# Performance work log

Measured on AMD Instinct MI355X. Metric: run time of the kernel, lower is better.

## Reference

```python
import jax, jax.numpy as jnp
import numpy as np

S, B, D, H = 256, 32, 512, 512

def setup_inputs() -> dict:
    key = jax.random.key(0)
    ks = jax.random.split(key, 14)
    return {
        "x": jax.random.normal(ks[0], (S, B, D), jnp.float32),
        "hidden_prev": jax.random.normal(ks[1], (1, B, H), jnp.float32) * 0.1,
        "Z_state": jax.random.normal(ks[2], (1, B, H, D), jnp.float32) * 0.01,
        "F_state": jax.random.normal(ks[3], (1, B, H, D), jnp.float32) * 0.01,
        "wz_state": jax.random.normal(ks[4], (1, B, H), jnp.float32) * 0.01,
        "wf_state": jax.random.normal(ks[5], (1, B, H), jnp.float32) * 0.01,
        "bz_state": jax.random.normal(ks[6], (1, B, H), jnp.float32) * 0.01,
        "bf_state": jax.random.normal(ks[7], (1, B, H), jnp.float32) * 0.01,
        "wm_z": jax.random.normal(ks[8], (H, D), jnp.float32) * 0.1,
        "wm_f": jax.random.normal(ks[9], (H, D), jnp.float32) * 0.1,
        "wv_z": jax.random.normal(ks[10], (1, H), jnp.float32) * 0.1,
        "wv_f": jax.random.normal(ks[11], (1, H), jnp.float32) * 0.1,
        "bias_z": jax.random.normal(ks[12], (1, H), jnp.float32) * 0.1,
        "bias_f": jax.random.normal(ks[13], (1, H), jnp.float32) * 0.1,
    }

def reference(x, hidden_prev, Z_state, F_state, wz_state, wf_state, bz_state, bf_state,
              wm_z, wm_f, wv_z, wv_f, bias_z, bias_f):
    # Input projections for both gates, done once: [S,B,H]
    pre_z = jnp.einsum('sbd,hd->sbh', x, wm_z)
    pre_f = jnp.einsum('sbd,hd->sbh', x, wm_f)

    def step(carry, inp):
        cell, Z, Fm, wz, wf, bz, bf = carry
        x_t, pz, pf = inp  # [B,D], [B,H], [B,H]
        z = jnp.tanh(pz + wv_z * cell + bias_z)          # [B,H]
        f = jax.nn.sigmoid(pf + wv_f * cell + bias_f)    # [B,H]
        zf = (1.0 - f) * (1.0 - z * z)
        fz = (cell - z) * (1.0 - f) * f
        common = f + zf * wv_z + fz * wv_f
        # RTRL sensitivity updates (outer products over [B,H,D])
        Zn = common[..., None] * Z + zf[..., None] * x_t[:, None, :]
        Fn = common[..., None] * Fm + fz[..., None] * x_t[:, None, :]
        wzn = cell * zf + common * wz
        wfn = cell * fz + common * wf
        bzn = zf + common * bz
        bfn = fz + common * bf
        new_cell = cell * f + (1.0 - f) * z
        return (new_cell, Zn, Fn, wzn, wfn, bzn, bfn), new_cell

    carry0 = (hidden_prev[0], Z_state[0], F_state[0],
              wz_state[0], wf_state[0], bz_state[0], bf_state[0])
    carry, cells = jax.lax.scan(step, carry0, (x, pre_z, pre_f))
    new_cell, Zn, Fn, wzn, wfn, bzn, bfn = carry
    return (cells, new_cell[None], Zn[None], Fn[None],
            wzn[None], wfn[None], bzn[None], bfn[None])
```

## Files before the change

kernel.cpp:

```cpp
#include <hip/hip_runtime.h>
#include <hip/hip_bf16.h>
#include <math.h>

namespace {

typedef short short8 __attribute__((ext_vector_type(8)));
typedef float floatx4 __attribute__((ext_vector_type(4)));
typedef unsigned int uint32;
typedef unsigned short u16;
typedef unsigned long long u64;

constexpr int S = 256, B = 32, D = 512, H = 512;
constexpr int BH = B * H;
constexpr int M1 = S * B;
constexpr int SBH = S * BH;

__device__ __forceinline__ int swz(int row, int col8) {
  return row * 64 + (col8 ^ ((row & 7) << 3));
}

__device__ __forceinline__ uint32 pkbf(float lo, float hi) {
  __hip_bfloat162 h = __float22bfloat162_rn(make_float2(lo, hi));
  uint32 r;
  __builtin_memcpy(&r, &h, 4);
  return r;
}

__device__ __forceinline__ float fast_sigmoid(float x) {
  float e = __expf(-x);
  return __builtin_amdgcn_rcpf(1.0f + e);
}
__device__ __forceinline__ float fast_tanh(float x) {
  float e = __expf(-2.0f * x);
  return fmaf(2.0f, __builtin_amdgcn_rcpf(1.0f + e), -1.0f);
}

__global__ __launch_bounds__(256) void proj_gemm(
    const float* __restrict__ x, const float* __restrict__ wmz,
    const float* __restrict__ wmf, float2* __restrict__ pzf) {
  __shared__ u16 As[128 * 64];
  __shared__ u16 Bzs[64 * 64];
  __shared__ u16 Bfs[64 * 64];
  const int tid = threadIdx.x;
  const int m0 = blockIdx.x * 128;
  const int n0 = blockIdx.y * 64;
  const int w = tid >> 6, l = tid & 63;
  const int lr = l & 15, lg = l >> 4;
  floatx4 accz[2][4], accf[2][4];
#pragma unroll
  for (int m = 0; m < 2; ++m)
#pragma unroll
    for (int n = 0; n < 4; ++n) {
      accz[m][n] = 0;
      accf[m][n] = 0;
    }
  const int sr = tid >> 3;
  const int sc = (tid & 7) * 8;
  for (int k0 = 0; k0 < D; k0 += 64) {
    __syncthreads();
#pragma unroll
    for (int p = 0; p < 4; ++p) {
      const int r = sr + 32 * p;
      const float* xp = &x[(size_t)(m0 + r) * D + k0 + sc];
      float4 a = *(const float4*)xp;
      float4 b = *(const float4*)(xp + 4);
      uint4 o;
      o.x = pkbf(a.x, a.y);
      o.y = pkbf(a.z, a.w);
      o.z = pkbf(b.x, b.y);
      o.w = pkbf(b.z, b.w);
      *(uint4*)&As[swz(r, sc)] = o;
    }
#pragma unroll
    for (int p = 0; p < 2; ++p) {
      const int r = sr + 32 * p;
      const float* zp = &wmz[(size_t)(n0 + r) * D + k0 + sc];
      float4 a = *(const float4*)zp;
      float4 b = *(const float4*)(zp + 4);
      uint4 o;
      o.x = pkbf(a.x, a.y);
      o.y = pkbf(a.z, a.w);
      o.z = pkbf(b.x, b.y);
      o.w = pkbf(b.z, b.w);
      *(uint4*)&Bzs[swz(r, sc)] = o;
      const float* fp = &wmf[(size_t)(n0 + r) * D + k0 + sc];
      float4 c = *(const float4*)fp;
      float4 d = *(const float4*)(fp + 4);
      uint4 q;
      q.x = pkbf(c.x, c.y);
      q.y = pkbf(c.z, c.w);
      q.z = pkbf(d.x, d.y);
      q.w = pkbf(d.z, d.w);
      *(uint4*)&Bfs[swz(r, sc)] = q;
    }
    __syncthreads();
    __builtin_amdgcn_s_setprio(1);
#pragma unroll
    for (int kk = 0; kk < 2; ++kk) {
      const int kb = kk * 32 + lg * 8;
      short8 a0 = *(const short8*)&As[swz(32 * w + lr, kb)];
      short8 a1 = *(const short8*)&As[swz(32 * w + 16 + lr, kb)];
#pragma unroll
      for (int n = 0; n < 4; ++n) {
        short8 bz = *(const short8*)&Bzs[swz(16 * n + lr, kb)];
        short8 bf = *(const short8*)&Bfs[swz(16 * n + lr, kb)];
        accz[0][n] = __builtin_amdgcn_mfma_f32_16x16x32_bf16(a0, bz, accz[0][n], 0, 0, 0);
        accz[1][n] = __builtin_amdgcn_mfma_f32_16x16x32_bf16(a1, bz, accz[1][n], 0, 0, 0);
        accf[0][n] = __builtin_amdgcn_mfma_f32_16x16x32_bf16(a0, bf, accf[0][n], 0, 0, 0);
        accf[1][n] = __builtin_amdgcn_mfma_f32_16x16x32_bf16(a1, bf, accf[1][n], 0, 0, 0);
      }
    }
    __builtin_amdgcn_s_setprio(0);
  }
#pragma unroll
  for (int m = 0; m < 2; ++m)
#pragma unroll
    for (int n = 0; n < 4; ++n)
#pragma unroll
      for (int j = 0; j < 4; ++j) {
        int row = m0 + 32 * w + 16 * m + lg * 4 + j;
        int col = n0 + 16 * n + lr;
        pzf[(size_t)row * H + col] = make_float2(accz[m][n][j], accf[m][n][j]);
      }
}

#define STEP_BODY(J)                                                       \
    const float z = fast_tanh(fmaf(wvz, cell, pzv));                       \
    const float f = fast_sigmoid(fmaf(wvf, cell, pfv));                    \
    const float zf = (1.0f - f) * (1.0f - z * z);                          \
    const float fz = (cell - z) * (1.0f - f) * f;                          \
    const float common = f + zf * wvz + fz * wvf;                          \
    wz = fmaf(common, wz, cell * zf);                                      \
    wf = fmaf(common, wf, cell * fz);                                      \
    bz = fmaf(common, bz, zf);                                             \
    bf = fmaf(common, bf, fz);                                             \
    cell = fmaf(f, cell - z, z);                                           \
    const size_t ti = (size_t)(t0 + (J)) * BH;                             \
    cp[ti] = cell;                                                         \
    pz[ti] = make_float2(__uint_as_float(pkbf(zf, fz)), common);

#define STEP_L(J, Q)                                                       \
  {                                                                        \
    const float pzv = Q.x + bsz, pfv = Q.y + bsf;                          \
    Q = pz[(size_t)(t0 + 16 + (J)) * BH];                                  \
    STEP_BODY(J)                                                           \
  }

#define STEP_N(J, Q)                                                       \
  {                                                                        \
    const float pzv = Q.x + bsz, pfv = Q.y + bsf;                          \
    STEP_BODY(J)                                                           \
  }

__global__ __launch_bounds__(64, 1) void scan_fwd(
    const float* __restrict__ hidden_prev, const float* __restrict__ wz0,
    const float* __restrict__ wf0, const float* __restrict__ bz0,
    const float* __restrict__ bf0, const float* __restrict__ wvz_,
    const float* __restrict__ wvf_, const float* __restrict__ bsz_,
    const float* __restrict__ bsf_, float2* pzf_,
    float* __restrict__ out_cells, float* __restrict__ out_newcell,
    float* __restrict__ out_wzn, float* __restrict__ out_wfn,
    float* __restrict__ out_bzn, float* __restrict__ out_bfn) {
  const int bh = blockIdx.x * 64 + threadIdx.x;
  const int h = bh & (H - 1);
  float cell = hidden_prev[bh];
  float wz = wz0[bh], wf = wf0[bh], bz = bz0[bh], bf = bf0[bh];
  const float wvz = wvz_[h], wvf = wvf_[h], bsz = bsz_[h], bsf = bsf_[h];
  float2* pz = pzf_ + bh;
  float* cp = out_cells + bh;

  float2 q0 = pz[(size_t)0 * BH], q1 = pz[(size_t)1 * BH];
  float2 q2 = pz[(size_t)2 * BH], q3 = pz[(size_t)3 * BH];
  float2 q4 = pz[(size_t)4 * BH], q5 = pz[(size_t)5 * BH];
  float2 q6 = pz[(size_t)6 * BH], q7 = pz[(size_t)7 * BH];
  float2 q8 = pz[(size_t)8 * BH], q9 = pz[(size_t)9 * BH];
  float2 q10 = pz[(size_t)10 * BH], q11 = pz[(size_t)11 * BH];
  float2 q12 = pz[(size_t)12 * BH], q13 = pz[(size_t)13 * BH];
  float2 q14 = pz[(size_t)14 * BH], q15 = pz[(size_t)15 * BH];

  for (int t0 = 0; t0 < S - 16; t0 += 16) {
    STEP_L(0, q0)  STEP_L(1, q1)  STEP_L(2, q2)  STEP_L(3, q3)
    STEP_L(4, q4)  STEP_L(5, q5)  STEP_L(6, q6)  STEP_L(7, q7)
    STEP_L(8, q8)  STEP_L(9, q9)  STEP_L(10, q10) STEP_L(11, q11)
    STEP_L(12, q12) STEP_L(13, q13) STEP_L(14, q14) STEP_L(15, q15)
  }
  {
    const int t0 = S - 16;
    STEP_N(0, q0)  STEP_N(1, q1)  STEP_N(2, q2)  STEP_N(3, q3)
    STEP_N(4, q4)  STEP_N(5, q5)  STEP_N(6, q6)  STEP_N(7, q7)
    STEP_N(8, q8)  STEP_N(9, q9)  STEP_N(10, q10) STEP_N(11, q11)
    STEP_N(12, q12) STEP_N(13, q13) STEP_N(14, q14) STEP_N(15, q15)
  }
  out_newcell[bh] = cell;
  out_wzn[bh] = wz;
  out_wfn[bh] = wf;
  out_bzn[bh] = bz;
  out_bfn[bh] = bf;
}

__global__ __launch_bounds__(1024) void suffix_kernel(
    const float2* __restrict__ pzfc, const float* __restrict__ x,
    u16* __restrict__ XT, u16* __restrict__ AzT, u16* __restrict__ AfT,
    float* __restrict__ P0_out) {
  __shared__ union {
    struct {
      float prods[16][65];
      uint32 tl[S * 65];
    } s;
    float xp[4][64][65];
  } u;
  const int tid = threadIdx.x;
  const int bh_l = tid & 63;
  const int c = tid >> 6;

  {
    const int team = tid >> 8;
    const int tt = tid & 255;
    const int tile = blockIdx.x * 4 + team;
    const int b = tile >> 5;
    const int rem = tile & 31;
    const int d0 = (rem >> 2) * 64;
    const int s0 = (rem & 3) * 64;
    const int r = tt >> 4;
    const int c4 = (tt & 15) * 4;
#pragma unroll
    for (int p = 0; p < 4; ++p) {
      const int rr = r + p * 16;
      float4 v = *(const float4*)&x[(size_t)(s0 + rr) * (B * D) +
                                    (size_t)b * D + d0 + c4];
      u.xp[team][c4 + 0][rr] = v.x;
      u.xp[team][c4 + 1][rr] = v.y;
      u.xp[team][c4 + 2][rr] = v.z;
      u.xp[team][c4 + 3][rr] = v.w;
    }
    __syncthreads();
#pragma unroll
    for (int p = 0; p < 4; ++p) {
      const int dr = r + p * 16;
      u64 o = (u64)pkbf(u.xp[team][dr][c4 + 0], u.xp[team][dr][c4 + 1]) |
              ((u64)pkbf(u.xp[team][dr][c4 + 2], u.xp[team][dr][c4 + 3]) << 32);
      *(u64*)&XT[((size_t)b * D + d0 + dr) * S + s0 + c4] = o;
    }
  }
  __syncthreads();

  const int bh = blockIdx.x * 64 + bh_l;
  const float2* p = pzfc + bh;
  float2 v[16];
#pragma unroll
  for (int i = 0; i < 16; ++i) v[i] = p[(size_t)(c * 16 + i) * BH];
  float L = 1.0f;
#pragma unroll
  for (int i = 0; i < 16; ++i) L *= v[i].y;
  u.s.prods[c][bh_l] = L;
  __syncthreads();
  float run = 1.0f;
#pragma unroll
  for (int cc = 1; cc < 16; ++cc)
    if (cc > c) run *= u.s.prods[cc][bh_l];
#pragma unroll
  for (int i = 15; i >= 0; --i) {
    const int t = c * 16 + i;
    const uint32 w32 = __float_as_uint(v[i].x);
    const float zf = __uint_as_float((w32 & 0xffffu) << 16);
    const float fz = __uint_as_float(w32 & 0xffff0000u);
    u.s.tl[t * 65 + bh_l] = pkbf(zf * run, fz * run);
    run *= v[i].y;
  }
  if (c == 0) P0_out[bh] = run;
  __syncthreads();

  const size_t base = (size_t)blockIdx.x * 64 * S;
  const int rot = (bh_l >> 3) & 3;
#pragma unroll
  for (int it = 0; it < 4; ++it) {
    const int qi = it * 1024 + tid;
    const int r = qi >> 6;
    const int qt = (qi & 63) * 4;
    uint32 a[4];
#pragma unroll
    for (int m = 0; m < 4; ++m) {
      const int k = (m + rot) & 3;
      a[k] = u.s.tl[(qt + k) * 65 + r];
    }
    u64 lo = (u64)(a[0] & 0xffffu) | ((u64)(a[1] & 0xffffu) << 16) |
             ((u64)(a[2] & 0xffffu) << 32) | ((u64)(a[3] & 0xffffu) << 48);
    u64 hi = (u64)(a[0] >> 16) | ((u64)(a[1] >> 16) << 16) |
             ((u64)(a[2] >> 16) << 32) | ((u64)(a[3] >> 16) << 48);
    *(u64*)&AzT[base + (size_t)r * S + qt] = lo;
    *(u64*)&AfT[base + (size_t)r * S + qt] = hi;
  }
}

__global__ __launch_bounds__(256, 3) void out_gemm(
    const u16* __restrict__ AzT, const u16* __restrict__ AfT,
    const u16* __restrict__ XT, const float* __restrict__ P0,
    const float* __restrict__ Z0, const float* __restrict__ F0,
    float* __restrict__ Zn, float* __restrict__ Fn) {
  __shared__ u16 smem[2][(128 + 64) * 64];
  const int tid = threadIdx.x;
  const int h0 = blockIdx.x * 128;
  const int d0 = blockIdx.y * 64;
  const int bz = blockIdx.z;
  const int b = bz >> 1;
  const u16* A = ((bz & 1) ? AfT : AzT) + (size_t)b * H * S;
  const float* C0 = (bz & 1) ? F0 : Z0;
  float* Cn = (bz & 1) ? Fn : Zn;
  const u16* Xb = XT + (size_t)b * D * S;
  const int w = tid >> 6, l = tid & 63;
  const int lr = l & 15, lg = l >> 4;
  floatx4 acc[2][4];
#pragma unroll
  for (int m = 0; m < 2; ++m)
#pragma unroll
    for (int n = 0; n < 4; ++n) acc[m][n] = 0;
  const int sr = tid >> 3;
  const int sc = (tid & 7) * 8;

  short8 rA[4], rX[2];

#define OG_LOAD(T0)                                                        \
  {                                                                        \
    _Pragma("unroll") for (int p = 0; p < 4; ++p) {                        \
      const int r = sr + 32 * p;                                           \
      rA[p] = *(const short8*)&A[(size_t)(h0 + r) * S + (T0) + sc];        \
    }                                                                      \
    _Pragma("unroll") for (int p = 0; p < 2; ++p) {                        \
      const int r = sr + 32 * p;                                           \
      rX[p] = *(const short8*)&Xb[(size_t)(d0 + r) * S + (T0) + sc];       \
    }                                                                      \
  }

#define OG_WRITE(BUF)                                                      \
  {                                                                        \
    u16* As_ = smem[BUF];                                                  \
    u16* Xs_ = smem[BUF] + 128 * 64;                                       \
    _Pragma("unroll") for (int p = 0; p < 4; ++p) {                        \
      const int r = sr + 32 * p;                                           \
      *(short8*)&As_[swz(r, sc)] = rA[p];                                  \
    }                                                                      \
    _Pragma("unroll") for (int p = 0; p < 2; ++p) {                        \
      const int r = sr + 32 * p;                                           \
      *(short8*)&Xs_[swz(r, sc)] = rX[p];                                  \
    }                                                                      \
  }

#define OG_COMPUTE(BUF)                                                    \
  {                                                                        \
    const u16* As_ = smem[BUF];                                            \
    const u16* Xs_ = smem[BUF] + 128 * 64;                                 \
    __builtin_amdgcn_s_setprio(1);                                         \
    _Pragma("unroll") for (int kk = 0; kk < 2; ++kk) {                     \
      const int kb = kk * 32 + lg * 8;                                     \
      short8 a0 = *(const short8*)&As_[swz(32 * w + lr, kb)];              \
      short8 a1 = *(const short8*)&As_[swz(32 * w + 16 + lr, kb)];         \
      _Pragma("unroll") for (int n = 0; n < 4; ++n) {                      \
        short8 xf = *(const short8*)&Xs_[swz(16 * n + lr, kb)];            \
        acc[0][n] = __builtin_amdgcn_mfma_f32_16x16x32_bf16(a0, xf, acc[0][n], 0, 0, 0); \
        acc[1][n] = __builtin_amdgcn_mfma_f32_16x16x32_bf16(a1, xf, acc[1][n], 0, 0, 0); \
      }                                                                    \
    }                                                                      \
    __builtin_amdgcn_s_setprio(0);                                         \
  }

  OG_LOAD(0)
  OG_WRITE(0)
  __syncthreads();
  OG_LOAD(64)
  OG_COMPUTE(0)
  OG_WRITE(1)
  __syncthreads();
  OG_LOAD(128)
  OG_COMPUTE(1)
  OG_WRITE(0)
  __syncthreads();
  OG_LOAD(192)
  OG_COMPUTE(0)
  OG_WRITE(1)
  __syncthreads();

  float4 c0v[8];
  float p0v[8];
#pragma unroll
  for (int i = 0; i < 8; ++i) {
    const int id = i * 256 + tid;
    const int row = id >> 4;
    const int c4 = (id & 15) * 4;
    const int h = h0 + row;
    p0v[i] = P0[b * H + h];
    c0v[i] = *(const float4*)&C0[((size_t)b * H + h) * D + d0 + c4];
  }

  OG_COMPUTE(1)

  __syncthreads();
  float* eps = (float*)&smem[0][0];
#pragma unroll
  for (int m = 0; m < 2; ++m)
#pragma unroll
    for (int n = 0; n < 4; ++n)
#pragma unroll
      for (int j = 0; j < 4; ++j) {
        const int row = 32 * w + 16 * m + lg * 4 + j;
        eps[row * 68 + 16 * n + lr] = acc[m][n][j];
      }
  __syncthreads();
#pragma unroll
  for (int i = 0; i < 8; ++i) {
    const int id = i * 256 + tid;
    const int row = id >> 4;
    const int c4 = (id & 15) * 4;
    const int h = h0 + row;
    const size_t gi = ((size_t)b * H + h) * D + d0 + c4;
    const float4 a = *(const float4*)&eps[row * 68 + c4];
    float4 o;
    o.x = fmaf(p0v[i], c0v[i].x, a.x);
    o.y = fmaf(p0v[i], c0v[i].y, a.y);
    o.z = fmaf(p0v[i], c0v[i].z, a.z);
    o.w = fmaf(p0v[i], c0v[i].w, a.w);
    *(float4*)&Cn[gi] = o;
  }
#undef OG_LOAD
#undef OG_WRITE
#undef OG_COMPUTE
}

}

extern "C" void kernel_launch(void* const* d_in, const int* in_sizes, int n_in,
                              void* d_out, int out_size, void* d_ws,
                              size_t ws_size, hipStream_t stream) {
  const float* x = (const float*)d_in[0];
  const float* hidden_prev = (const float*)d_in[1];
  const float* Z_state = (const float*)d_in[2];
  const float* F_state = (const float*)d_in[3];
  const float* wz_state = (const float*)d_in[4];
  const float* wf_state = (const float*)d_in[5];
  const float* bz_state = (const float*)d_in[6];
  const float* bf_state = (const float*)d_in[7];
  const float* wm_z = (const float*)d_in[8];
  const float* wm_f = (const float*)d_in[9];
  const float* wv_z = (const float*)d_in[10];
  const float* wv_f = (const float*)d_in[11];
  const float* bias_z = (const float*)d_in[12];
  const float* bias_f = (const float*)d_in[13];

  float2* pzf = (float2*)d_ws;
  u16* AzT = (u16*)(pzf + SBH);
  u16* AfT = AzT + SBH;
  u16* XT = AfT + SBH;
  float* P0 = (float*)(XT + SBH);

  float* out = (float*)d_out;
  float* out_cells = out;
  float* out_newcell = out + SBH;
  float* out_Zn = out_newcell + BH;
  float* out_Fn = out_Zn + (size_t)BH * D;
  float* out_wzn = out_Fn + (size_t)BH * D;
  float* out_wfn = out_wzn + BH;
  float* out_bzn = out_wfn + BH;
  float* out_bfn = out_bzn + BH;

  proj_gemm<<<dim3(M1 / 128, H / 64), 256, 0, stream>>>(x, wm_z, wm_f, pzf);
  scan_fwd<<<BH / 64, 64, 0, stream>>>(
      hidden_prev, wz_state, wf_state, bz_state, bf_state, wv_z, wv_f, bias_z,
      bias_f, pzf, out_cells, out_newcell, out_wzn, out_wfn, out_bzn,
      out_bfn);
  suffix_kernel<<<BH / 64, 1024, 0, stream>>>(pzf, x, XT, AzT, AfT, P0);
  out_gemm<<<dim3(H / 128, D / 64, B * 2), 256, 0, stream>>>(
      AzT, AfT, XT, P0, Z_state, F_state, out_Zn, out_Fn);
}
```

Before: 102.3 us.

## Single-buffer out_gemm shared memory and split epilogue staging in halves

The out_gemm kernel goes from a double-buffered LDS tile to a single buffer, which halves shared memory per block (about 48KB down to 24KB) and so allows more resident blocks per CU. Because only one buffer remains, an extra barrier is added between compute and the next LDS write, so writes no longer overlap the previous tile's reads. The epilogue now stages the fp32 accumulators through LDS in two 64-row halves so the staging area fits in the smaller buffer. The cost is more __syncthreads and less overlap within each block, traded for higher occupancy.

New measurement: 102.3 us. No clear change (+0.0%).

```diff
diff --git a/kernel.cpp b/kernel.cpp
--- a/kernel.cpp
+++ b/kernel.cpp
@@ -297,7 +297,7 @@
     const u16* __restrict__ XT, const float* __restrict__ P0,
     const float* __restrict__ Z0, const float* __restrict__ F0,
     float* __restrict__ Zn, float* __restrict__ Fn) {
-  __shared__ u16 smem[2][(128 + 64) * 64];
+  __shared__ u16 smem[(128 + 64) * 64];
   const int tid = threadIdx.x;
   const int h0 = blockIdx.x * 128;
   const int d0 = blockIdx.y * 64;
@@ -331,10 +331,10 @@
     }                                                                      \
   }
 
-#define OG_WRITE(BUF)                                                      \
+#define OG_WRITE()                                                         \
   {                                                                        \
-    u16* As_ = smem[BUF];                                                  \
-    u16* Xs_ = smem[BUF] + 128 * 64;                                       \
+    u16* As_ = smem;                                                       \
+    u16* Xs_ = smem + 128 * 64;                                            \
     _Pragma("unroll") for (int p = 0; p < 4; ++p) {                        \
       const int r = sr + 32 * p;                                           \
       *(short8*)&As_[swz(r, sc)] = rA[p];                                  \
@@ -345,10 +345,10 @@
     }                                                                      \
   }
 
-#define OG_COMPUTE(BUF)                                                    \
+#define OG_COMPUTE()                                                       \
   {                                                                        \
-    const u16* As_ = smem[BUF];                                            \
-    const u16* Xs_ = smem[BUF] + 128 * 64;                                 \
+    const u16* As_ = smem;                                                 \
+    const u16* Xs_ = smem + 128 * 64;                                      \
     __builtin_amdgcn_s_setprio(1);                                         \
     _Pragma("unroll") for (int kk = 0; kk < 2; ++kk) {                     \
       const int kb = kk * 32 + lg * 8;                                     \
@@ -364,61 +364,74 @@
   }
 
   OG_LOAD(0)
-  OG_WRITE(0)
+  OG_WRITE()
   __syncthreads();
   OG_LOAD(64)
-  OG_COMPUTE(0)
-  OG_WRITE(1)
+  OG_COMPUTE()
+  __syncthreads();
+  OG_WRITE()
   __syncthreads();
   OG_LOAD(128)
-  OG_COMPUTE(1)
-  OG_WRITE(0)
+  OG_COMPUTE()
+  __syncthreads();
+  OG_WRITE()
   __syncthreads();
   OG_LOAD(192)
-  OG_COMPUTE(0)
-  OG_WRITE(1)
+  OG_COMPUTE()
+  __syncthreads();
+  OG_WRITE()
   __syncthreads();
 
   float4 c0v[8];
   float p0v[8];
 #pragma unroll
-  for (int i = 0; i < 8; ++i) {
-    const int id = i * 256 + tid;
-    const int row = id >> 4;
-    const int c4 = (id & 15) * 4;
-    const int h = h0 + row;
-    p0v[i] = P0[b * H + h];
-    c0v[i] = *(const float4*)&C0[((size_t)b * H + h) * D + d0 + c4];
-  }
-
-  OG_COMPUTE(1)
-
-  __syncthreads();
-  float* eps = (float*)&smem[0][0];
-#pragma unroll
-  for (int m = 0; m < 2; ++m)
-#pragma unroll
-    for (int n = 0; n < 4; ++n)
-#pragma unroll
-      for (int j = 0; j < 4; ++j) {
-        const int row = 32 * w + 16 * m + lg * 4 + j;
-        eps[row * 68 + 16 * n + lr] = acc[m][n][j];
-      }
-  __syncthreads();
-#pragma unroll
-  for (int i = 0; i < 8; ++i) {
-    const int id = i * 256 + tid;
-    const int row = id >> 4;
-    const int c4 = (id & 15) * 4;
-    const int h = h0 + row;
-    const size_t gi = ((size_t)b * H + h) * D + d0 + c4;
-    const float4 a = *(const float4*)&eps[row * 68 + c4];
-    float4 o;
-    o.x = fmaf(p0v[i], c0v[i].x, a.x);
-    o.y = fmaf(p0v[i], c0v[i].y, a.y);
-    o.z = fmaf(p0v[i], c0v[i].z, a.z);
-    o.w = fmaf(p0v[i], c0v[i].w, a.w);
-    *(float4*)&Cn[gi] = o;
+  for (int half = 0; half < 2; ++half)
+#pragma unroll
+    for (int i = 0; i < 4; ++i) {
+      const int id = i * 256 + tid;
+      const int row = half * 64 + (id >> 4);
+      const int c4 = (id & 15) * 4;
+      const int h = h0 + row;
+      p0v[half * 4 + i] = P0[b * H + h];
+      c0v[half * 4 + i] =
+          *(const float4*)&C0[((size_t)b * H + h) * D + d0 + c4];
+    }
+
+  OG_COMPUTE()
+
+  float* eps = (float*)smem;
+#pragma unroll
+  for (int half = 0; half < 2; ++half) {
+    __syncthreads();
+    if ((w >> 1) == half) {
+      const int lw = w & 1;
+#pragma unroll
+      for (int m = 0; m < 2; ++m)
+#pragma unroll
+        for (int n = 0; n < 4; ++n)
+#pragma unroll
+          for (int j = 0; j < 4; ++j) {
+            const int row = 32 * lw + 16 * m + lg * 4 + j;
+            eps[row * 68 + 16 * n + lr] = acc[m][n][j];
+          }
+    }
+    __syncthreads();
+#pragma unroll
+    for (int i = 0; i < 4; ++i) {
+      const int id = i * 256 + tid;
+      const int row = id >> 4;
+      const int c4 = (id & 15) * 4;
+      const int h = h0 + half * 64 + row;
+      const size_t gi = ((size_t)b * H + h) * D + d0 + c4;
+      const float4 a = *(const float4*)&eps[row * 68 + c4];
+      const int pi = half * 4 + i;
+      float4 o;
+      o.x = fmaf(p0v[pi], c0v[pi].x, a.x);
+      o.y = fmaf(p0v[pi], c0v[pi].y, a.y);
+      o.z = fmaf(p0v[pi], c0v[pi].z, a.z);
+      o.w = fmaf(p0v[pi], c0v[pi].w, a.w);
+      *(float4*)&Cn[gi] = o;
+    }
   }
 #undef OG_LOAD
 #undef OG_WRITE
```
